# Optimization experiments

Measured on AMD Instinct MI355X. Metric: run time of the kernel, lower is better.

The kernel has to match this reference:

```python
import jax, jax.numpy as jnp
import numpy as np

H = 12          # heads (longformer-base)
DH = 64         # head dim
W = 256         # one-sided window (attention_window=512 in HF convention)


def _heads(t, B, S):
    return t.reshape(B, S, H, DH).transpose(0, 2, 1, 3)  # [B,H,S,dh]


def _forward(x, mask, clss, emb, pos, wq, wk, wv, wo, wqg, wkg, wvg):
    B, S = x.shape
    D = emb.shape[1]
    h = emb[x] + pos[None, :S]                      # [B,S,D]

    scale = DH ** -0.5
    q = _heads(h @ wq, B, S) * scale                # [B,H,S,dh]
    k = _heads(h @ wk, B, S)
    v = _heads(h @ wv, B, S)

    # ---- sliding-window (banded) attention, chunked like HF ----
    nc = S // W
    kpos = (jnp.arange(nc) * W - W)[:, None] + jnp.arange(3 * W)[None, :]   # [nc,3w] absolute key pos
    kidx = kpos + W                                  # index into padded seq
    kp = jnp.pad(k, ((0, 0), (0, 0), (W, W), (0, 0)))
    vp = jnp.pad(v, ((0, 0), (0, 0), (W, W), (0, 0)))
    Kc = kp[:, :, kidx, :]                           # [B,H,nc,3w,dh]
    Vc = vp[:, :, kidx, :]
    Qc = q.reshape(B, H, nc, W, DH)
    band = jnp.einsum('bhcqd,bhckd->bhcqk', Qc, Kc)  # [B,H,nc,w,3w]

    qpos = (jnp.arange(nc) * W)[:, None] + jnp.arange(W)[None, :]           # [nc,w]
    rel = kpos[:, None, :] - qpos[:, :, None]                               # [nc,w,3w]
    inband = (rel >= -W) & (rel <= W) & (kpos[:, None, :] >= 0) & (kpos[:, None, :] < S)

    is_global = jnp.zeros((S,), bool).at[clss].set(True)
    kpos_c = jnp.clip(kpos, 0, S - 1)
    # global keys are handled via dedicated columns, so remove them from the band (as HF does)
    key_ok = (mask[:, kpos_c] != 0) & (~is_global[kpos_c])                  # [B,nc,3w]

    NEG = jnp.finfo(band.dtype).min
    m = inband[None, None] & key_ok[:, None, :, None, :]                    # [B,H,nc,w,3w]
    band = jnp.where(m, band, NEG)
    band_flat = band.reshape(B, H, S, 3 * W)

    # ---- local queries attending to global keys ----
    kg_loc = k[:, :, clss, :]                        # [B,H,G,dh]
    vg_loc = v[:, :, clss, :]
    sg = jnp.einsum('bhsd,bhgd->bhsg', q, kg_loc)
    gm = (mask[:, clss] != 0)[:, None, None, :]
    sg = jnp.where(gm, sg, NEG)

    scores = jnp.concatenate([band_flat, sg], axis=-1)   # [B,H,S,3w+G]
    probs = jax.nn.softmax(scores, axis=-1)
    p_band = probs[..., : 3 * W].reshape(B, H, nc, W, 3 * W)
    p_g = probs[..., 3 * W:]
    out = jnp.einsum('bhcqk,bhckd->bhcqd', p_band, Vc).reshape(B, H, S, DH)
    out = out + jnp.einsum('bhsg,bhgd->bhsd', p_g, vg_loc)

    # ---- global queries: full attention with separate global projections ----
    qg = _heads(h @ wqg, B, S)[:, :, clss, :] * scale    # [B,H,G,dh]
    kg = _heads(h @ wkg, B, S)
    vg = _heads(h @ wvg, B, S)
    sgg = jnp.einsum('bhgd,bhsd->bhgs', qg, kg)
    sgg = jnp.where((mask != 0)[:, None, None, :], sgg, NEG)
    og = jnp.einsum('bhgs,bhsd->bhgd', jax.nn.softmax(sgg, axis=-1), vg)
    out = out.at[:, :, clss, :].set(og)

    top_vec = out.transpose(0, 2, 1, 3).reshape(B, S, D) @ wo
    return top_vec


def setup_inputs() -> dict:
    key = jax.random.key(0)
    ks = jax.random.split(key, 12)
    B, S, D, V, G = 2, 4096, 768, 50265, 64
    std = 0.02
    x = jax.random.randint(ks[0], (B, S), 0, V)
    mask = jnp.ones((B, S), jnp.int32)
    clss = jnp.sort(jax.random.randint(ks[1], (G,), 0, S))
    emb = jax.random.normal(ks[2], (V, D), jnp.float32) * std
    pos = jax.random.normal(ks[3], (S, D), jnp.float32) * std
    wq = jax.random.normal(ks[4], (D, D), jnp.float32) * std
    wk = jax.random.normal(ks[5], (D, D), jnp.float32) * std
    wv = jax.random.normal(ks[6], (D, D), jnp.float32) * std
    wo = jax.random.normal(ks[7], (D, D), jnp.float32) * std
    wqg = jax.random.normal(ks[8], (D, D), jnp.float32) * std
    wkg = jax.random.normal(ks[9], (D, D), jnp.float32) * std
    wvg = jax.random.normal(ks[10], (D, D), jnp.float32) * std
    return {"x": x, "mask": mask, "clss": clss, "emb": emb, "pos": pos,
            "wq": wq, "wk": wk, "wv": wv, "wo": wo,
            "wqg": wqg, "wkg": wkg, "wvg": wvg}


def reference(x, mask, clss, emb, pos, wq, wk, wv, wo, wqg, wkg, wvg):
    return _forward(x, mask, clss, emb, pos, wq, wk, wv, wo, wqg, wkg, wvg)
```

## Files before the change

### kernel.cpp

```cpp
#include <hip/hip_runtime.h>
#include <stdint.h>

typedef unsigned short u16;
typedef unsigned char u8;
typedef unsigned int u32;
typedef __attribute__((ext_vector_type(8))) short short8x;
typedef __attribute__((ext_vector_type(4))) float f32x4;
typedef __attribute__((ext_vector_type(16))) float f32x16;

#define DEV static __device__ __forceinline__

DEV u16 f2bf(float f) {
  union { float f; unsigned u; } v; v.f = f;
  unsigned r = v.u + 0x7FFFu + ((v.u >> 16) & 1u);
  return (u16)(r >> 16);
}
DEV int imin(int a, int b) { return a < b ? a : b; }
DEV int imax(int a, int b) { return a > b ? a : b; }
DEV float ex2(float x) { return __builtin_exp2f(x); }

DEV void gload16(const void* g, void* l) {
  __builtin_amdgcn_global_load_lds((const __attribute__((address_space(1))) void*)g,
                                   (__attribute__((address_space(3))) void*)l, 16, 0, 0);
}

DEV u32 cvtpk_bf16(float lo, float hi) {
  u32 r;
  asm("v_cvt_pk_bf16_f32 %0, %1, %2" : "=v"(r) : "v"(lo), "v"(hi));
  return r;
}
DEV void plswap(u32& a, u32& b) {
  asm("v_permlane32_swap_b32 %0, %1" : "+v"(a), "+v"(b));
}

#define LOG2E 1.44269504f

struct WPtrs { const float* p[7]; };

__global__ __launch_bounds__(256) void wconv_kernel(WPtrs wp, u16* __restrict__ wt) {
  const int mat = blockIdx.y;
  const int kt = blockIdx.x % 12, nt = blockIdx.x / 12;
  const float* __restrict__ w = wp.p[mat];
  __shared__ float tile[64][72];
  const int t = threadIdx.x;
  {
    const int kk = t >> 2, n0 = (t & 3) * 16;
    const float* src = w + (size_t)(kt * 64 + kk) * 768 + nt * 64 + n0;
#pragma unroll
    for (int i = 0; i < 4; ++i)
      *(float4*)&tile[kk][n0 + i * 4] = *(const float4*)(src + i * 4);
  }
  __syncthreads();
  {
    const int nn = t >> 2, k0 = (t & 3) * 16;
    u16* dst = wt + (size_t)(mat * 768 + nt * 64 + nn) * 768 + kt * 64 + k0;
    short8x v0, v1;
#pragma unroll
    for (int j = 0; j < 8; ++j) {
      v0[j] = (short)f2bf(tile[k0 + j][nn]);
      v1[j] = (short)f2bf(tile[k0 + 8 + j][nn]);
    }
    *(short8x*)dst = v0;
    *(short8x*)(dst + 8) = v1;
  }
}

__global__ __launch_bounds__(256) void embed_kernel(const int* __restrict__ x, const float* __restrict__ emb,
                                                    const float* __restrict__ pos, u16* __restrict__ hb) {
  const int n4 = 2 * 4096 * 192;
  for (int i = blockIdx.x * 256 + threadIdx.x; i < n4; i += gridDim.x * 256) {
    const int r = i / 192;
    const int d4 = i - r * 192;
    const int s = r & 4095;
    const int tok = x[r];
    const float4 e = *(const float4*)(emb + (size_t)tok * 768 + d4 * 4);
    const float4 p = *(const float4*)(pos + (size_t)s * 768 + d4 * 4);
    union { u16 u[4]; uint2 v; } o;
    o.u[0] = f2bf(e.x + p.x);
    o.u[1] = f2bf(e.y + p.y);
    o.u[2] = f2bf(e.z + p.z);
    o.u[3] = f2bf(e.w + p.w);
    *(uint2*)(hb + (size_t)r * 768 + d4 * 4) = o.v;
  }
}

__global__ __launch_bounds__(256) void bits_kernel(const int* __restrict__ clss, const int* __restrict__ mask,
                                                   u32* __restrict__ kv32, u32* __restrict__ mv32,
                                                   u32* __restrict__ mc32) {
  __shared__ u8 isg[4096];
  const int t = threadIdx.x;
  for (int i = t; i < 4096; i += 256) isg[i] = 0;
  __syncthreads();
  if (t < 64) isg[clss[t]] = 1;
  __syncthreads();
  {
    const int b = t >> 7, i = t & 127;
    u32 kv = 0, mvv = 0;
    for (int j = 0; j < 32; ++j) {
      const int key = i * 32 + j;
      const u32 m = (u32)(mask[b * 4096 + key] != 0);
      mvv |= m << j;
      kv |= (m & (u32)(isg[key] == 0)) << j;
    }
    kv32[b * 128 + i] = kv;
    mv32[b * 128 + i] = mvv;
  }
  if (t < 4) {
    const int b = t >> 1, wi = t & 1;
    u32 mc = 0;
    for (int j = 0; j < 32; ++j) {
      const int g = wi * 32 + j;
      mc |= (u32)(mask[b * 4096 + clss[g]] != 0) << j;
    }
    mc32[b * 2 + wi] = mc;
  }
}

__global__ __launch_bounds__(256) void hgather_kernel(const u16* __restrict__ hb, const int* __restrict__ clss,
                                                      u16* __restrict__ hg) {
  const int i = blockIdx.x * 256 + threadIdx.x;
  const int r = i / 96, c8 = i - r * 96;
  const int b = r >> 6, g = r & 63;
  const int s = clss[g];
  *(short8x*)(hg + (size_t)r * 768 + c8 * 8) =
      *(const short8x*)(hb + ((size_t)b * 4096 + s) * 768 + c8 * 8);
}

struct Outs6 { u16* p[6]; };

template <int MODE>
__global__ __launch_bounds__(256) void gemm_kernel(const u16* __restrict__ A, const u16* __restrict__ Bt,
                                                   Outs6 outs, float* __restrict__ outF) {
  __shared__ __align__(16) u16 smA[2][128 * 64];
  __shared__ __align__(16) u16 smB[2][128 * 64];
  const int t = threadIdx.x;
  const int l = t & 63, w = t >> 6;
  const int l15 = l & 15, grp = l >> 4;
  const int wm = w >> 1, wn = w & 1;
  int bx = blockIdx.x, by = blockIdx.y;
  if (MODE == 0) {
    int id = blockIdx.x;
    id = (id & 7) * 240 + (id >> 3);
    bx = id % 30;
    by = id / 30;
  }
  const int m0 = by * 128, n0 = bx * 128;
  const f32x4 zero4 = {0.f, 0.f, 0.f, 0.f};
  f32x4 acc[4][4];
#pragma unroll
  for (int mi = 0; mi < 4; ++mi)
#pragma unroll
    for (int ni = 0; ni < 4; ++ni) acc[mi][ni] = zero4;

  const int sr = l >> 3;
  const int scb = (l & 7) * 16;

  auto STAGE = [&](int kb, int d) {
#pragma unroll
    for (int c = 0; c < 4; ++c) {
      const int rg = w * 4 + c;
      const int r = rg * 8 + sr;
      const int sc = scb ^ (((r >> 2) & 3) << 5);
      gload16(A + (size_t)(m0 + r) * 768 + kb * 64 + (sc >> 1), (char*)smA[d] + rg * 1024);
      gload16(Bt + (size_t)(n0 + r) * 768 + kb * 64 + (sc >> 1), (char*)smB[d] + rg * 1024);
    }
  };
  const int xorf = ((l15 >> 2) & 3) << 5;
  auto RDA = [&](int d, int mi, int kk) {
    return *(const short8x*)((const char*)smA[d] + (wm * 64 + mi * 16 + l15) * 128 + ((kk * 64 + grp * 16) ^ xorf));
  };
  auto RDB = [&](int d, int ni, int kk) {
    return *(const short8x*)((const char*)smB[d] + (wn * 64 + ni * 16 + l15) * 128 + ((kk * 64 + grp * 16) ^ xorf));
  };

  STAGE(0, 0);
  STAGE(1, 1);
  asm volatile("s_waitcnt vmcnt(8)" ::: "memory");
  __builtin_amdgcn_s_barrier();
  __builtin_amdgcn_sched_barrier(0);

  short8x a0[4], b0[4], a1[4], b1[4];
#pragma unroll
  for (int i = 0; i < 4; ++i) { a0[i] = RDA(0, i, 0); b0[i] = RDB(0, i, 0); }

  for (int kt = 0; kt < 12; ++kt) {
    const int cur = kt & 1;
#pragma unroll
    for (int i = 0; i < 4; ++i) { a1[i] = RDA(cur, i, 1); b1[i] = RDB(cur, i, 1); }
    __builtin_amdgcn_s_setprio(1);
#pragma unroll
    for (int mi = 0; mi < 4; ++mi)
#pragma unroll
      for (int ni = 0; ni < 4; ++ni)
        acc[mi][ni] = __builtin_amdgcn_mfma_f32_16x16x32_bf16(a0[mi], b0[ni], acc[mi][ni], 0, 0, 0);
    __builtin_amdgcn_s_setprio(0);
    if (kt < 11) {
      asm volatile("s_waitcnt lgkmcnt(0)" ::: "memory");
      __builtin_amdgcn_s_barrier();
      __builtin_amdgcn_sched_barrier(0);
      if (kt < 10) {
        STAGE(kt + 2, cur);
        asm volatile("s_waitcnt vmcnt(8)" ::: "memory");
      } else {
        asm volatile("s_waitcnt vmcnt(0)" ::: "memory");
      }
      __builtin_amdgcn_s_barrier();
      __builtin_amdgcn_sched_barrier(0);
#pragma unroll
      for (int i = 0; i < 4; ++i) { a0[i] = RDA(cur ^ 1, i, 0); b0[i] = RDB(cur ^ 1, i, 0); }
    }
    __builtin_amdgcn_s_setprio(1);
#pragma unroll
    for (int mi = 0; mi < 4; ++mi)
#pragma unroll
      for (int ni = 0; ni < 4; ++ni)
        acc[mi][ni] = __builtin_amdgcn_mfma_f32_16x16x32_bf16(a1[mi], b1[ni], acc[mi][ni], 0, 0, 0);
    __builtin_amdgcn_s_setprio(0);
  }

  if (MODE == 0) {
    const int mat = bx / 6;
    const int inn0 = n0 - mat * 768 + wn * 64;
    u16* __restrict__ base = outs.p[mat];
    if (mat == 2 || mat == 4) {
#pragma unroll
      for (int mi = 0; mi < 4; ++mi) {
        const int row0 = m0 + wm * 64 + mi * 16 + grp * 4;
        const int b = row0 >> 12, s = row0 & 4095;
#pragma unroll
        for (int ni = 0; ni < 4; ++ni) {
          const int col = inn0 + ni * 16 + l15;
          const int hd = col >> 6, dh = col & 63;
          union { u16 u[4]; uint2 v; } o;
#pragma unroll
          for (int rr = 0; rr < 4; ++rr) o.u[rr] = f2bf(acc[mi][ni][rr]);
          *(uint2*)(base + ((size_t)(b * 12 + hd) * 64 + dh) * 4096 + s) = o.v;
        }
      }
    } else {
      const float scl = (mat == 0) ? 0.125f * LOG2E : 1.0f;
#pragma unroll
      for (int mi = 0; mi < 4; ++mi)
#pragma unroll
        for (int ni = 0; ni < 4; ++ni) {
          const int col = inn0 + ni * 16 + l15;
          const int hd = col >> 6, dh = col & 63;
#pragma unroll
          for (int rr = 0; rr < 4; ++rr) {
            const int row = m0 + wm * 64 + mi * 16 + grp * 4 + rr;
            const int b = row >> 12, s = row & 4095;
            base[((size_t)(b * 12 + hd) * 4096 + s) * 64 + dh] = f2bf(acc[mi][ni][rr] * scl);
          }
        }
    }
  } else if (MODE == 1) {
#pragma unroll
    for (int mi = 0; mi < 4; ++mi)
#pragma unroll
      for (int rr = 0; rr < 4; ++rr) {
        const int row = m0 + wm * 64 + mi * 16 + grp * 4 + rr;
#pragma unroll
        for (int ni = 0; ni < 4; ++ni) {
          const int col = n0 + wn * 64 + ni * 16 + l15;
          outF[(size_t)row * 768 + col] = acc[mi][ni][rr];
        }
      }
  } else {
    u16* __restrict__ base = outs.p[0];
#pragma unroll
    for (int mi = 0; mi < 4; ++mi)
#pragma unroll
      for (int ni = 0; ni < 4; ++ni) {
        const int col = n0 + wn * 64 + ni * 16 + l15;
        const int hd = col >> 6, dh = col & 63;
#pragma unroll
        for (int rr = 0; rr < 4; ++rr) {
          const int row = wm * 64 + mi * 16 + grp * 4 + rr;
          const int b = row >> 6, g = row & 63;
          base[((size_t)(b * 12 + hd) * 64 + g) * 64 + dh] = f2bf(acc[mi][ni][rr] * 0.125f * LOG2E);
        }
      }
  }
}

__global__ __launch_bounds__(256) void gcls_kernel(const u16* __restrict__ kB, const u16* __restrict__ vTs,
                                                   const int* __restrict__ clss,
                                                   u16* __restrict__ kcls, u16* __restrict__ vtcls) {
  const int bh = blockIdx.x;
  __shared__ int sc[64];
  const int t = threadIdx.x;
  if (t < 64) sc[t] = clss[t];
  __syncthreads();
  {
    const int g = t >> 2, d0 = (t & 3) * 16;
    const int row = sc[g];
    const u16* pk = kB + ((size_t)bh * 4096 + row) * 64 + d0;
    u16* ok = kcls + ((size_t)bh * 64 + g) * 64 + d0;
    *(short8x*)ok = *(const short8x*)pk;
    *(short8x*)(ok + 8) = *(const short8x*)(pk + 8);
  }
  {
    const int dh = t >> 2, g0 = (t & 3) * 16;
    const u16* vrow = vTs + ((size_t)bh * 64 + dh) * 4096;
    short8x v0, v1;
#pragma unroll
    for (int j = 0; j < 8; ++j) {
      v0[j] = (short)vrow[sc[g0 + j]];
      v1[j] = (short)vrow[sc[g0 + 8 + j]];
    }
    u16* o = vtcls + ((size_t)bh * 64 + dh) * 64 + g0;
    *(short8x*)o = v0;
    *(short8x*)(o + 8) = v1;
  }
}

struct AttnState {
  f32x16 a0, a1;
  float m, l;
};

#define ATTN_SOFTMAX_PV(S, s0, s1, vm0, vm1, LOADV0, LOADV1)                        \
  {                                                                                  \
    float mx[8];                                                                     \
    _Pragma("unroll") for (int e = 0; e < 8; ++e)                                    \
        mx[e] = fmaxf(fmaxf(s0[e], s0[e + 8]), fmaxf(s1[e], s1[e + 8]));             \
    mx[0] = fmaxf(mx[0], mx[4]); mx[1] = fmaxf(mx[1], mx[5]);                        \
    mx[2] = fmaxf(mx[2], mx[6]); mx[3] = fmaxf(mx[3], mx[7]);                        \
    mx[0] = fmaxf(mx[0], mx[2]); mx[1] = fmaxf(mx[1], mx[3]);                        \
    float mv = fmaxf(mx[0], mx[1]);                                                  \
    mv = fmaxf(mv, __shfl_xor(mv, 32));                                              \
    if (!__all(mv <= S.m + 8.f)) {                                                   \
      const float mn = fmaxf(S.m, mv);                                               \
      const float sc = ex2(S.m - mn);                                                \
      S.m = mn; S.l *= sc;                                                           \
      _Pragma("unroll") for (int e = 0; e < 16; ++e) { S.a0[e] *= sc; S.a1[e] *= sc; } \
    }                                                                                \
    float p0[16], p1[16];                                                            \
    if ((vm0 & vm1) == 0xFFFFFFFFu) {                                                \
      _Pragma("unroll") for (int e = 0; e < 16; ++e) {                               \
        p0[e] = ex2(s0[e] - S.m); p1[e] = ex2(s1[e] - S.m);                          \
      }                                                                              \
    } else {                                                                         \
      const u32 w0 = vm0 >> (hf * 4), w1 = vm1 >> (hf * 4);                          \
      _Pragma("unroll") for (int e = 0; e < 16; ++e) {                               \
        const int cr = (e & 3) + 8 * (e >> 2);                                       \
        p0[e] = ex2(s0[e] - S.m) * (float)((w0 >> cr) & 1u);                         \
        p1[e] = ex2(s1[e] - S.m) * (float)((w1 >> cr) & 1u);                         \
      }                                                                              \
    }                                                                                \
    float sm[8];                                                                     \
    _Pragma("unroll") for (int e = 0; e < 8; ++e)                                    \
        sm[e] = (p0[e] + p0[e + 8]) + (p1[e] + p1[e + 8]);                           \
    sm[0] += sm[4]; sm[1] += sm[5]; sm[2] += sm[6]; sm[3] += sm[7];                  \
    sm[0] += sm[2]; sm[1] += sm[3];                                                  \
    float ls = sm[0] + sm[1];                                                        \
    ls += __shfl_xor(ls, 32);                                                        \
    S.l += ls;                                                                       \
    _Pragma("unroll") for (int st = 0; st < 2; ++st) {                               \
      const float* pp = st ? p1 : p0;                                                \
      _Pragma("unroll") for (int c = 0; c < 2; ++c) {                                \
        u32 A1 = cvtpk_bf16(pp[8 * c + 0], pp[8 * c + 1]);                           \
        u32 A2 = cvtpk_bf16(pp[8 * c + 2], pp[8 * c + 3]);                           \
        u32 B1 = cvtpk_bf16(pp[8 * c + 4], pp[8 * c + 5]);                           \
        u32 B2 = cvtpk_bf16(pp[8 * c + 6], pp[8 * c + 7]);                           \
        plswap(A1, B1); plswap(A2, B2);                                              \
        union { u32 w[4]; short8x v; } u;                                            \
        u.w[0] = A1; u.w[1] = A2; u.w[2] = B1; u.w[3] = B2;                          \
        const int sc4 = st * 2 + c;                                                  \
        const short8x vf0 = LOADV0(sc4);                                             \
        const short8x vf1 = LOADV1(sc4);                                             \
        S.a0 = __builtin_amdgcn_mfma_f32_32x32x16_bf16(vf0, u.v, S.a0, 0, 0, 0);     \
        S.a1 = __builtin_amdgcn_mfma_f32_32x32x16_bf16(vf1, u.v, S.a1, 0, 0, 0);     \
      }                                                                              \
    }                                                                                \
  }

DEV void attn_tile64(const u16* __restrict__ kp, const u16* __restrict__ vp, int vstr,
                     u32 vm0, u32 vm1, const short8x* qf, AttnState& S, int l31, int hf) {
  const int h8 = hf * 8;
  const f32x16 z16 = {0.f};
  f32x16 s0 = z16, s1 = z16;
  const u16* kr0 = kp + (size_t)l31 * 64 + h8;
  const u16* kr1 = kr0 + 32 * 64;
#pragma unroll
  for (int ks = 0; ks < 4; ++ks) {
    const short8x kf0 = *(const short8x*)(kr0 + ks * 16);
    const short8x kf1 = *(const short8x*)(kr1 + ks * 16);
    s0 = __builtin_amdgcn_mfma_f32_32x32x16_bf16(kf0, qf[ks], s0, 0, 0, 0);
    s1 = __builtin_amdgcn_mfma_f32_32x32x16_bf16(kf1, qf[ks], s1, 0, 0, 0);
  }
#define LV0(sc4) (*(const short8x*)(vp + (sc4) * 16 + h8 + (size_t)l31 * vstr))
#define LV1(sc4) (*(const short8x*)(vp + (sc4) * 16 + h8 + (size_t)(32 + l31) * vstr))
  ATTN_SOFTMAX_PV(S, s0, s1, vm0, vm1, LV0, LV1)
#undef LV0
#undef LV1
}

DEV void attn_tile64_lds(const char* __restrict__ Kl, const char* __restrict__ Vl,
                         u32 vm0, u32 vm1, const short8x* qf, AttnState& S, int l31, int hf) {
  const int swz = (l31 & 7) << 4;
  const f32x16 z16 = {0.f};
  f32x16 s0 = z16, s1 = z16;
#pragma unroll
  for (int ks = 0; ks < 4; ++ks) {
    const int cb = (hf * 16 + ks * 32) ^ swz;
    const short8x kf0 = *(const short8x*)(Kl + l31 * 128 + cb);
    const short8x kf1 = *(const short8x*)(Kl + (32 + l31) * 128 + cb);
    s0 = __builtin_amdgcn_mfma_f32_32x32x16_bf16(kf0, qf[ks], s0, 0, 0, 0);
    s1 = __builtin_amdgcn_mfma_f32_32x32x16_bf16(kf1, qf[ks], s1, 0, 0, 0);
  }
#define LV0(sc4) (*(const short8x*)(Vl + l31 * 128 + (((sc4) * 32 + hf * 16) ^ swz)))
#define LV1(sc4) (*(const short8x*)(Vl + (32 + l31) * 128 + (((sc4) * 32 + hf * 16) ^ swz)))
  ATTN_SOFTMAX_PV(S, s0, s1, vm0, vm1, LV0, LV1)
#undef LV0
#undef LV1
}

DEV u32 bandmask32(int q, int kb2) {
  const int lo = imax(q - 256 - kb2, 0);
  const int hi = imin(q + 256 - kb2, 31);
  if (hi < lo) return 0u;
  return (0xFFFFFFFFu << lo) & (0xFFFFFFFFu >> (31 - hi));
}

struct FusedArgs {
  const u16 *qB, *kB, *vT, *kcls, *vtcls, *qgc, *kgB, *vgT;
  const u32 *kv32, *mv32, *mc32;
  u16* aout;
  float *pm, *pl, *pacc;
};

__global__ __launch_bounds__(256, 3) void band_kernel(FusedArgs a) {
  const int t = threadIdx.x;
  const int w = t >> 6, l = t & 63;
  const int l31 = l & 31, hf = l >> 5, h4 = hf * 4;
  const f32x16 z16 = {0.f};

  __shared__ __align__(16) char Ktile[2][8192];
  __shared__ __align__(16) char Vtile[2][8192];

  if (blockIdx.x < 96) {
    const int wid = blockIdx.x * 4 + w;
    const int sl = wid & 7;
    const int qsub = (wid >> 3) & 1;
    const int bh = wid >> 4;
    const int b = bh / 12;
    const int q = qsub * 32 + l31;

    const u16* kgb = a.kgB + (size_t)bh * 4096 * 64;
    const u16* vgb = a.vgT + (size_t)bh * 64 * 4096;
    short8x qf[4];
#pragma unroll
    for (int ks = 0; ks < 4; ++ks)
      qf[ks] = *(const short8x*)(a.qgc + ((size_t)bh * 64 + q) * 64 + ks * 16 + hf * 8);

    AttnState S;
    S.a0 = z16; S.a1 = z16; S.m = -60.f; S.l = 0.f;
    for (int tt = sl * 8; tt < sl * 8 + 8; ++tt) {
      const int kb = tt * 64;
      const u32 vm0 = a.mv32[b * 128 + tt * 2];
      const u32 vm1 = a.mv32[b * 128 + tt * 2 + 1];
      attn_tile64(kgb + (size_t)kb * 64, vgb + kb, 4096, vm0, vm1, qf, S, l31, hf);
    }
    const int pbase = (bh * 8 + sl) * 64;
    float* pr = a.pacc + ((size_t)pbase + q) * 64;
#pragma unroll
    for (int rq = 0; rq < 4; ++rq) {
      f32x4 v0 = {S.a0[rq * 4 + 0], S.a0[rq * 4 + 1], S.a0[rq * 4 + 2], S.a0[rq * 4 + 3]};
      f32x4 v1 = {S.a1[rq * 4 + 0], S.a1[rq * 4 + 1], S.a1[rq * 4 + 2], S.a1[rq * 4 + 3]};
      *(f32x4*)(pr + rq * 8 + h4) = v0;
      *(f32x4*)(pr + 32 + rq * 8 + h4) = v1;
    }
    if (hf == 0) {
      a.pm[pbase + q] = S.m;
      a.pl[pbase + q] = S.l;
    }
    return;
  }

  int bid = blockIdx.x - 96;
  bid = (bid & 7) * 96 + (bid >> 3);
  const int qblk = bid & 31;
  const int h = (bid >> 5) % 12;
  const int b = bid / 384;
  const int bh = b * 12 + h;
  const int q0b = qblk * 128;
  const int q0w = q0b + w * 32;
  const int q = q0w + l31;

  const u16* kbh = a.kB + (size_t)bh * 4096 * 64;
  const u16* vbh = a.vT + (size_t)bh * 64 * 4096;
  const u16* kcb = a.kcls + (size_t)bh * 4096;
  const u16* vcb = a.vtcls + (size_t)bh * 4096;

  short8x qf[4];
#pragma unroll
  for (int ks = 0; ks < 4; ++ks)
    qf[ks] = *(const short8x*)(a.qB + ((size_t)bh * 4096 + q) * 64 + ks * 16 + hf * 8);

  AttnState S;
  S.a0 = z16; S.a1 = z16; S.m = -60.f; S.l = 0.f;

  const int tloB = imax(0, q0b - 256) >> 6;
  const int thiB = imin(63, (q0b + 383) >> 6);
  const int nB = thiB - tloB + 1;
  const int tlo_w = (imax(0, q0w - 256) >> 6) - tloB;
  const int thi_w = (imin(63, (q0w + 287) >> 6)) - tloB;

  auto STAGE = [&](const u16* ksrc, const u16* vsrc, int vstr, int buf) {
#pragma unroll
    for (int c = 0; c < 2; ++c) {
      const int rw = w + 4 * c;
      const int row = rw * 8 + (l >> 3);
      const int seg = (l & 7) ^ (row & 7);
      gload16(ksrc + (size_t)row * 64 + seg * 8, Ktile[buf] + rw * 1024);
      gload16(vsrc + (size_t)row * vstr + seg * 8, Vtile[buf] + rw * 1024);
    }
  };

  STAGE(kbh + (size_t)tloB * 64 * 64, vbh + (size_t)tloB * 64, 4096, 0);
  __syncthreads();

  for (int i = 0; i <= nB; ++i) {
    const int buf = i & 1;
    if (i < nB) {
      if (i + 1 == nB) STAGE(kcb, vcb, 64, buf ^ 1);
      else             STAGE(kbh + (size_t)(tloB + i + 1) * 64 * 64,
                             vbh + (size_t)(tloB + i + 1) * 64, 4096, buf ^ 1);
    }
    const bool isG = (i == nB);
    if (isG || (i >= tlo_w && i <= thi_w)) {
      u32 vm0, vm1;
      if (isG) {
        vm0 = a.mc32[b * 2];
        vm1 = a.mc32[b * 2 + 1];
      } else {
        const int tt = tloB + i;
        const int kb = tt * 64;
        vm0 = a.kv32[b * 128 + tt * 2];
        vm1 = a.kv32[b * 128 + tt * 2 + 1];
        const int d0 = kb - q0w, d1 = kb + 32 - q0w;
        if (d0 < -225 || d0 > 225) vm0 &= bandmask32(q, kb);
        if (d1 < -225 || d1 > 225) vm1 &= bandmask32(q, kb + 32);
      }
      attn_tile64_lds(Ktile[buf], Vtile[buf], vm0, vm1, qf, S, l31, hf);
    }
    __syncthreads();
  }

  const float inv = 1.f / S.l;
  u16* ob = a.aout + ((size_t)b * 4096 + q) * 768 + h * 64;
#pragma unroll
  for (int rq = 0; rq < 4; ++rq) {
    union { u16 s[4]; uint2 v; } o0, o1;
#pragma unroll
    for (int j = 0; j < 4; ++j) {
      o0.s[j] = f2bf(S.a0[rq * 4 + j] * inv);
      o1.s[j] = f2bf(S.a1[rq * 4 + j] * inv);
    }
    *(uint2*)(ob + rq * 8 + h4) = o0.v;
    *(uint2*)(ob + 32 + rq * 8 + h4) = o1.v;
  }
}

__global__ __launch_bounds__(256) void ogm_kernel(const float* __restrict__ pm, const float* __restrict__ pl,
                                                  const float* __restrict__ pacc, const int* __restrict__ clss,
                                                  u16* __restrict__ aout) {
  const int bh = blockIdx.x;
  const int b = bh / 12, h = bh % 12;
  const int t = threadIdx.x;
  const int r = t >> 2, cs = (t & 3) * 16;
  float mv[8];
  float M = -1e30f;
#pragma unroll
  for (int s = 0; s < 8; ++s) {
    mv[s] = pm[(bh * 8 + s) * 64 + r];
    M = fmaxf(M, mv[s]);
  }
  float L = 0.f, f[8];
#pragma unroll
  for (int s = 0; s < 8; ++s) {
    f[s] = ex2(mv[s] - M);
    L += pl[(bh * 8 + s) * 64 + r] * f[s];
  }
  float o[16];
#pragma unroll
  for (int j = 0; j < 16; ++j) o[j] = 0.f;
#pragma unroll
  for (int s = 0; s < 8; ++s) {
    const float* pr = pacc + (size_t)(bh * 8 + s) * 4096 + r * 64 + cs;
#pragma unroll
    for (int j4 = 0; j4 < 4; ++j4) {
      const float4 a = *(const float4*)(pr + j4 * 4);
      o[j4 * 4 + 0] += a.x * f[s];
      o[j4 * 4 + 1] += a.y * f[s];
      o[j4 * 4 + 2] += a.z * f[s];
      o[j4 * 4 + 3] += a.w * f[s];
    }
  }
  const float inv = 1.f / L;
  short8x v0, v1;
#pragma unroll
  for (int j = 0; j < 8; ++j) {
    v0[j] = (short)f2bf(o[j] * inv);
    v1[j] = (short)f2bf(o[8 + j] * inv);
  }
  u16* op = aout + ((size_t)b * 4096 + clss[r]) * 768 + h * 64 + cs;
  *(short8x*)op = v0;
  *(short8x*)(op + 8) = v1;
}

extern "C" void kernel_launch(void* const* d_in, const int* in_sizes, int n_in,
                              void* d_out, int out_size, void* d_ws, size_t ws_size,
                              hipStream_t stream) {
  (void)in_sizes; (void)n_in; (void)out_size; (void)ws_size;
  const int* x = (const int*)d_in[0];
  const int* mask = (const int*)d_in[1];
  const int* clss = (const int*)d_in[2];
  const float* emb = (const float*)d_in[3];
  const float* pos = (const float*)d_in[4];
  const float* wq = (const float*)d_in[5];
  const float* wk = (const float*)d_in[6];
  const float* wv = (const float*)d_in[7];
  const float* wo = (const float*)d_in[8];
  const float* wqg = (const float*)d_in[9];
  const float* wkg = (const float*)d_in[10];
  const float* wvg = (const float*)d_in[11];
  float* out = (float*)d_out;

  char* ws = (char*)d_ws;
  size_t off = 0;
  auto alloc = [&](size_t n) { char* p = ws + off; off = (off + n + 255) & ~(size_t)255; return p; };
  const size_t SZ = (size_t)2 * 12 * 4096 * 64 * 2;
  u16* hb = (u16*)alloc(SZ);
  u16* wt = (u16*)alloc((size_t)7 * 768 * 768 * 2);
  u16* qb = (u16*)alloc(SZ);
  u16* kb = (u16*)alloc(SZ);
  u16* kgb = (u16*)alloc(SZ);
  u16* vts = (u16*)alloc(SZ);
  u16* vgts = (u16*)alloc(SZ);
  u16* hg = (u16*)alloc((size_t)128 * 768 * 2);
  u16* qgc = (u16*)alloc((size_t)24 * 64 * 64 * 2);
  u16* kcls = (u16*)alloc((size_t)24 * 64 * 64 * 2);
  u16* vtcls = (u16*)alloc((size_t)24 * 64 * 64 * 2);
  u32* kv32 = (u32*)alloc(256 * 4);
  u32* mv32 = (u32*)alloc(256 * 4);
  u32* mc32 = (u32*)alloc(4 * 4);
  u16* aout = (u16*)alloc(SZ);
  float* pm = (float*)alloc((size_t)192 * 64 * 4);
  float* pl = (float*)alloc((size_t)192 * 64 * 4);
  float* pacc = (float*)alloc((size_t)192 * 4096 * 4);

  WPtrs wp;
  wp.p[0] = wq; wp.p[1] = wk; wp.p[2] = wv; wp.p[3] = wkg; wp.p[4] = wvg; wp.p[5] = wqg; wp.p[6] = wo;

  wconv_kernel<<<dim3(144, 7), 256, 0, stream>>>(wp, wt);
  embed_kernel<<<2048, 256, 0, stream>>>(x, emb, pos, hb);
  bits_kernel<<<1, 256, 0, stream>>>(clss, mask, kv32, mv32, mc32);

  Outs6 o5;
  o5.p[0] = qb; o5.p[1] = kb; o5.p[2] = vts; o5.p[3] = kgb; o5.p[4] = vgts; o5.p[5] = nullptr;
  gemm_kernel<0><<<1920, 256, 0, stream>>>(hb, wt, o5, nullptr);

  hgather_kernel<<<48, 256, 0, stream>>>(hb, clss, hg);
  Outs6 oq = {};
  oq.p[0] = qgc;
  gemm_kernel<2><<<dim3(6, 1), 256, 0, stream>>>(hg, wt + (size_t)5 * 768 * 768, oq, nullptr);

  gcls_kernel<<<24, 256, 0, stream>>>(kb, vts, clss, kcls, vtcls);

  FusedArgs fa;
  fa.qB = qb; fa.kB = kb; fa.vT = vts; fa.kcls = kcls; fa.vtcls = vtcls;
  fa.qgc = qgc; fa.kgB = kgb; fa.vgT = vgts;
  fa.kv32 = kv32; fa.mv32 = mv32; fa.mc32 = mc32;
  fa.aout = aout; fa.pm = pm; fa.pl = pl; fa.pacc = pacc;
  band_kernel<<<864, 256, 0, stream>>>(fa);

  ogm_kernel<<<24, 256, 0, stream>>>(pm, pl, pacc, clss, aout);

  Outs6 dummy = {};
  gemm_kernel<1><<<dim3(6, 64), 256, 0, stream>>>(aout, wt + (size_t)6 * 768 * 768, dummy, out);
}
```

Before: 184.9 us.

## Merge prep kernels into one launch and fold global-query GEMM into QKV GEMM

The weight conversion, embedding, mask-bit and global-row gather kernels are combined into one prep kernel that dispatches work by block index. The global rows are now computed directly from the embedding instead of being gathered from hb. The small global-query projection GEMM is appended as six extra blocks of the main QKV GEMM launch. This cuts four kernel launches and the serialization between them, at the cost of branchier kernels and some recomputed embedding rows.

```diff
diff --git a/kernel.cpp b/kernel.cpp
--- a/kernel.cpp
+++ b/kernel.cpp
@@ -37,42 +37,98 @@
 
 struct WPtrs { const float* p[7]; };
 
-__global__ __launch_bounds__(256) void wconv_kernel(WPtrs wp, u16* __restrict__ wt) {
-  const int mat = blockIdx.y;
-  const int kt = blockIdx.x % 12, nt = blockIdx.x / 12;
-  const float* __restrict__ w = wp.p[mat];
-  __shared__ float tile[64][72];
+__global__ __launch_bounds__(256) void prep_kernel(
+    WPtrs wp, const int* __restrict__ x, const float* __restrict__ emb,
+    const float* __restrict__ pos, const int* __restrict__ clss,
+    const int* __restrict__ mask, u16* __restrict__ wt, u16* __restrict__ hb,
+    u16* __restrict__ hg, u32* __restrict__ kv32, u32* __restrict__ mv32,
+    u32* __restrict__ mc32) {
+  __shared__ __align__(16) char smraw[64 * 72 * 4];
+  const int bid = blockIdx.x;
   const int t = threadIdx.x;
+
+  if (bid < 1008) {
+    const int mat = bid / 144;
+    const int inner = bid - mat * 144;
+    const int kt = inner % 12, nt = inner / 12;
+    const float* __restrict__ w = wp.p[mat];
+    float(*tile)[72] = (float(*)[72])smraw;
+    {
+      const int kk = t >> 2, n0 = (t & 3) * 16;
+      const float* src = w + (size_t)(kt * 64 + kk) * 768 + nt * 64 + n0;
+#pragma unroll
+      for (int i = 0; i < 4; ++i)
+        *(float4*)&tile[kk][n0 + i * 4] = *(const float4*)(src + i * 4);
+    }
+    __syncthreads();
+    {
+      const int nn = t >> 2, k0 = (t & 3) * 16;
+      u16* dst = wt + (size_t)(mat * 768 + nt * 64 + nn) * 768 + kt * 64 + k0;
+      short8x v0, v1;
+#pragma unroll
+      for (int j = 0; j < 8; ++j) {
+        v0[j] = (short)f2bf(tile[k0 + j][nn]);
+        v1[j] = (short)f2bf(tile[k0 + 8 + j][nn]);
+      }
+      *(short8x*)dst = v0;
+      *(short8x*)(dst + 8) = v1;
+    }
+    return;
+  }
+  if (bid < 2032) {
+    const int vb = bid - 1008;
+    const int n4 = 2 * 4096 * 192;
+    for (int i = vb * 256 + t; i < n4; i += 1024 * 256) {
+      const int r = i / 192;
+      const int d4 = i - r * 192;
+      const int s = r & 4095;
+      const int tok = x[r];
+      const float4 e = *(const float4*)(emb + (size_t)tok * 768 + d4 * 4);
+      const float4 p = *(const float4*)(pos + (size_t)s * 768 + d4 * 4);
+      union { u16 u[4]; uint2 v; } o;
+      o.u[0] = f2bf(e.x + p.x);
+      o.u[1] = f2bf(e.y + p.y);
+      o.u[2] = f2bf(e.z + p.z);
+      o.u[3] = f2bf(e.w + p.w);
+      *(uint2*)(hb + (size_t)r * 768 + d4 * 4) = o.v;
+    }
+    return;
+  }
+  if (bid == 2032) {
+    u8* isg = (u8*)smraw;
+    for (int i = t; i < 4096; i += 256) isg[i] = 0;
+    __syncthreads();
+    if (t < 64) isg[clss[t]] = 1;
+    __syncthreads();
+    {
+      const int b = t >> 7, i = t & 127;
+      u32 kv = 0, mvv = 0;
+      for (int j = 0; j < 32; ++j) {
+        const int key = i * 32 + j;
+        const u32 m = (u32)(mask[b * 4096 + key] != 0);
+        mvv |= m << j;
+        kv |= (m & (u32)(isg[key] == 0)) << j;
+      }
+      kv32[b * 128 + i] = kv;
+      mv32[b * 128 + i] = mvv;
+    }
+    if (t < 4) {
+      const int b = t >> 1, wi = t & 1;
+      u32 mc = 0;
+      for (int j = 0; j < 32; ++j) {
+        const int g = wi * 32 + j;
+        mc |= (u32)(mask[b * 4096 + clss[g]] != 0) << j;
+      }
+      mc32[b * 2 + wi] = mc;
+    }
+    return;
+  }
   {
-    const int kk = t >> 2, n0 = (t & 3) * 16;
-    const float* src = w + (size_t)(kt * 64 + kk) * 768 + nt * 64 + n0;
-#pragma unroll
-    for (int i = 0; i < 4; ++i)
-      *(float4*)&tile[kk][n0 + i * 4] = *(const float4*)(src + i * 4);
-  }
-  __syncthreads();
-  {
-    const int nn = t >> 2, k0 = (t & 3) * 16;
-    u16* dst = wt + (size_t)(mat * 768 + nt * 64 + nn) * 768 + kt * 64 + k0;
-    short8x v0, v1;
-#pragma unroll
-    for (int j = 0; j < 8; ++j) {
-      v0[j] = (short)f2bf(tile[k0 + j][nn]);
-      v1[j] = (short)f2bf(tile[k0 + 8 + j][nn]);
-    }
-    *(short8x*)dst = v0;
-    *(short8x*)(dst + 8) = v1;
-  }
-}
-
-__global__ __launch_bounds__(256) void embed_kernel(const int* __restrict__ x, const float* __restrict__ emb,
-                                                    const float* __restrict__ pos, u16* __restrict__ hb) {
-  const int n4 = 2 * 4096 * 192;
-  for (int i = blockIdx.x * 256 + threadIdx.x; i < n4; i += gridDim.x * 256) {
-    const int r = i / 192;
-    const int d4 = i - r * 192;
-    const int s = r & 4095;
-    const int tok = x[r];
+    const int i = (bid - 2033) * 256 + t;
+    const int r = i / 192, d4 = i - r * 192;
+    const int b = r >> 6, g = r & 63;
+    const int s = clss[g];
+    const int tok = x[b * 4096 + s];
     const float4 e = *(const float4*)(emb + (size_t)tok * 768 + d4 * 4);
     const float4 p = *(const float4*)(pos + (size_t)s * 768 + d4 * 4);
     union { u16 u[4]; uint2 v; } o;
@@ -80,56 +136,15 @@
     o.u[1] = f2bf(e.y + p.y);
     o.u[2] = f2bf(e.z + p.z);
     o.u[3] = f2bf(e.w + p.w);
-    *(uint2*)(hb + (size_t)r * 768 + d4 * 4) = o.v;
-  }
-}
-
-__global__ __launch_bounds__(256) void bits_kernel(const int* __restrict__ clss, const int* __restrict__ mask,
-                                                   u32* __restrict__ kv32, u32* __restrict__ mv32,
-                                                   u32* __restrict__ mc32) {
-  __shared__ u8 isg[4096];
-  const int t = threadIdx.x;
-  for (int i = t; i < 4096; i += 256) isg[i] = 0;
-  __syncthreads();
-  if (t < 64) isg[clss[t]] = 1;
-  __syncthreads();
-  {
-    const int b = t >> 7, i = t & 127;
-    u32 kv = 0, mvv = 0;
-    for (int j = 0; j < 32; ++j) {
-      const int key = i * 32 + j;
-      const u32 m = (u32)(mask[b * 4096 + key] != 0);
-      mvv |= m << j;
-      kv |= (m & (u32)(isg[key] == 0)) << j;
-    }
-    kv32[b * 128 + i] = kv;
-    mv32[b * 128 + i] = mvv;
-  }
-  if (t < 4) {
-    const int b = t >> 1, wi = t & 1;
-    u32 mc = 0;
-    for (int j = 0; j < 32; ++j) {
-      const int g = wi * 32 + j;
-      mc |= (u32)(mask[b * 4096 + clss[g]] != 0) << j;
-    }
-    mc32[b * 2 + wi] = mc;
-  }
-}
-
-__global__ __launch_bounds__(256) void hgather_kernel(const u16* __restrict__ hb, const int* __restrict__ clss,
-                                                      u16* __restrict__ hg) {
-  const int i = blockIdx.x * 256 + threadIdx.x;
-  const int r = i / 96, c8 = i - r * 96;
-  const int b = r >> 6, g = r & 63;
-  const int s = clss[g];
-  *(short8x*)(hg + (size_t)r * 768 + c8 * 8) =
-      *(const short8x*)(hb + ((size_t)b * 4096 + s) * 768 + c8 * 8);
+    *(uint2*)(hg + (size_t)r * 768 + d4 * 4) = o.v;
+  }
 }
 
 struct Outs6 { u16* p[6]; };
 
 template <int MODE>
 __global__ __launch_bounds__(256) void gemm_kernel(const u16* __restrict__ A, const u16* __restrict__ Bt,
+                                                   const u16* __restrict__ A2, const u16* __restrict__ Bt2,
                                                    Outs6 outs, float* __restrict__ outF) {
   __shared__ __align__(16) u16 smA[2][128 * 64];
   __shared__ __align__(16) u16 smB[2][128 * 64];
@@ -138,12 +153,21 @@
   const int l15 = l & 15, grp = l >> 4;
   const int wm = w >> 1, wn = w & 1;
   int bx = blockIdx.x, by = blockIdx.y;
+  bool qg = false;
   if (MODE == 0) {
     int id = blockIdx.x;
-    id = (id & 7) * 240 + (id >> 3);
-    bx = id % 30;
-    by = id / 30;
-  }
+    if (id >= 1920) {
+      qg = true;
+      bx = id - 1920;
+      by = 0;
+    } else {
+      id = (id & 7) * 240 + (id >> 3);
+      bx = id % 30;
+      by = id / 30;
+    }
+  }
+  const u16* __restrict__ Ap = (MODE == 0 && qg) ? A2 : A;
+  const u16* __restrict__ Btp = (MODE == 0 && qg) ? Bt2 : Bt;
   const int m0 = by * 128, n0 = bx * 128;
   const f32x4 zero4 = {0.f, 0.f, 0.f, 0.f};
   f32x4 acc[4][4];
@@ -161,8 +185,8 @@
       const int rg = w * 4 + c;
       const int r = rg * 8 + sr;
       const int sc = scb ^ (((r >> 2) & 3) << 5);
-      gload16(A + (size_t)(m0 + r) * 768 + kb * 64 + (sc >> 1), (char*)smA[d] + rg * 1024);
-      gload16(Bt + (size_t)(n0 + r) * 768 + kb * 64 + (sc >> 1), (char*)smB[d] + rg * 1024);
+      gload16(Ap + (size_t)(m0 + r) * 768 + kb * 64 + (sc >> 1), (char*)smA[d] + rg * 1024);
+      gload16(Btp + (size_t)(n0 + r) * 768 + kb * 64 + (sc >> 1), (char*)smB[d] + rg * 1024);
     }
   };
   const int xorf = ((l15 >> 2) & 3) << 5;
@@ -219,6 +243,23 @@
   }
 
   if (MODE == 0) {
+    if (qg) {
+      u16* __restrict__ base = outs.p[5];
+#pragma unroll
+      for (int mi = 0; mi < 4; ++mi)
+#pragma unroll
+        for (int ni = 0; ni < 4; ++ni) {
+          const int col = n0 + wn * 64 + ni * 16 + l15;
+          const int hd = col >> 6, dh = col & 63;
+#pragma unroll
+          for (int rr = 0; rr < 4; ++rr) {
+            const int row = wm * 64 + mi * 16 + grp * 4 + rr;
+            const int b = row >> 6, g = row & 63;
+            base[((size_t)(b * 12 + hd) * 64 + g) * 64 + dh] = f2bf(acc[mi][ni][rr] * 0.125f * LOG2E);
+          }
+        }
+      return;
+    }
     const int mat = bx / 6;
     const int inn0 = n0 - mat * 768 + wn * 64;
     u16* __restrict__ base = outs.p[mat];
@@ -253,7 +294,7 @@
           }
         }
     }
-  } else if (MODE == 1) {
+  } else {
 #pragma unroll
     for (int mi = 0; mi < 4; ++mi)
 #pragma unroll
@@ -263,21 +304,6 @@
         for (int ni = 0; ni < 4; ++ni) {
           const int col = n0 + wn * 64 + ni * 16 + l15;
           outF[(size_t)row * 768 + col] = acc[mi][ni][rr];
-        }
-      }
-  } else {
-    u16* __restrict__ base = outs.p[0];
-#pragma unroll
-    for (int mi = 0; mi < 4; ++mi)
-#pragma unroll
-      for (int ni = 0; ni < 4; ++ni) {
-        const int col = n0 + wn * 64 + ni * 16 + l15;
-        const int hd = col >> 6, dh = col & 63;
-#pragma unroll
-        for (int rr = 0; rr < 4; ++rr) {
-          const int row = wm * 64 + mi * 16 + grp * 4 + rr;
-          const int b = row >> 6, g = row & 63;
-          base[((size_t)(b * 12 + hd) * 64 + g) * 64 + dh] = f2bf(acc[mi][ni][rr] * 0.125f * LOG2E);
         }
       }
   }
@@ -654,18 +680,11 @@
   WPtrs wp;
   wp.p[0] = wq; wp.p[1] = wk; wp.p[2] = wv; wp.p[3] = wkg; wp.p[4] = wvg; wp.p[5] = wqg; wp.p[6] = wo;
 
-  wconv_kernel<<<dim3(144, 7), 256, 0, stream>>>(wp, wt);
-  embed_kernel<<<2048, 256, 0, stream>>>(x, emb, pos, hb);
-  bits_kernel<<<1, 256, 0, stream>>>(clss, mask, kv32, mv32, mc32);
+  prep_kernel<<<2129, 256, 0, stream>>>(wp, x, emb, pos, clss, mask, wt, hb, hg, kv32, mv32, mc32);
 
   Outs6 o5;
-  o5.p[0] = qb; o5.p[1] = kb; o5.p[2] = vts; o5.p[3] = kgb; o5.p[4] = vgts; o5.p[5] = nullptr;
-  gemm_kernel<0><<<1920, 256, 0, stream>>>(hb, wt, o5, nullptr);
-
-  hgather_kernel<<<48, 256, 0, stream>>>(hb, clss, hg);
-  Outs6 oq = {};
-  oq.p[0] = qgc;
-  gemm_kernel<2><<<dim3(6, 1), 256, 0, stream>>>(hg, wt + (size_t)5 * 768 * 768, oq, nullptr);
+  o5.p[0] = qb; o5.p[1] = kb; o5.p[2] = vts; o5.p[3] = kgb; o5.p[4] = vgts; o5.p[5] = qgc;
+  gemm_kernel<0><<<1926, 256, 0, stream>>>(hb, wt, hg, wt + (size_t)5 * 768 * 768, o5, nullptr);
 
   gcls_kernel<<<24, 256, 0, stream>>>(kb, vts, clss, kcls, vtcls);
 
@@ -679,5 +698,5 @@
   ogm_kernel<<<24, 256, 0, stream>>>(pm, pl, pacc, clss, aout);
 
   Outs6 dummy = {};
-  gemm_kernel<1><<<dim3(6, 64), 256, 0, stream>>>(aout, wt + (size_t)6 * 768 * 768, dummy, out);
-}
+  gemm_kernel<1><<<dim3(6, 64), 256, 0, stream>>>(aout, wt + (size_t)6 * 768 * 768, nullptr, nullptr, dummy, out);
+}
```

Result: faster. 169.5 us (-8.3%).
